# Kernel optimization log

Measured on AMD Instinct MI355X. Metric: run time of the kernel, lower is better.

## Reference

```python
import jax, jax.numpy as jnp
import numpy as np

B, T, D, H = 8, 512, 1024, 16
DK = D // H  # 64
EPS = 1e-3  # Keras BatchNormalization default epsilon


def batchnorm(x, gamma, beta):
    # Keras BN over feature axis (-1), training-mode batch statistics over (B, T)
    mean = jnp.mean(x, axis=(0, 1), keepdims=True)
    var = jnp.var(x, axis=(0, 1), keepdims=True)
    return (x - mean) * jax.lax.rsqrt(var + EPS) * gamma + beta


def setup_inputs() -> dict:
    key = jax.random.key(0)
    ks = jax.random.split(key, 12)
    s = 0.05
    return {
        "x": jax.random.normal(ks[0], (B, T, D), dtype=jnp.float32),
        "Wq": jax.random.uniform(ks[1], (H, D, DK), dtype=jnp.float32, minval=-s, maxval=s),
        "Wk": jax.random.uniform(ks[2], (H, D, DK), dtype=jnp.float32, minval=-s, maxval=s),
        "Wv": jax.random.uniform(ks[3], (H, D, DK), dtype=jnp.float32, minval=-s, maxval=s),
        "W": jax.random.uniform(ks[4], (D, D), dtype=jnp.float32, minval=-s, maxval=s),
        "W1": jax.random.normal(ks[5], (D, D), dtype=jnp.float32) * 0.02,
        "b1": jnp.zeros((D,), dtype=jnp.float32),
        "W2": jax.random.normal(ks[6], (D, D), dtype=jnp.float32) * 0.02,
        "b2": jnp.zeros((D,), dtype=jnp.float32),
        "g1": jnp.ones((D,), dtype=jnp.float32),
        "be1": jnp.zeros((D,), dtype=jnp.float32),
        "g2": jnp.ones((D,), dtype=jnp.float32),
        "be2": jnp.zeros((D,), dtype=jnp.float32),
    }


def reference(x, Wq, Wk, Wv, W, W1, b1, W2, b2, g1, be1, g2, be2):
    # Batched multi-head attention (replaces the per-head Python loop)
    q = jnp.einsum("btd,hdk->bhtk", x, Wq)
    k = jnp.einsum("btd,hdk->bhtk", x, Wk)
    v = jnp.einsum("btd,hdk->bhtk", x, Wv)
    scores = jnp.einsum("bhtk,bhsk->bhts", q, k) / jnp.sqrt(jnp.float32(DK))
    w = jax.nn.softmax(scores, axis=-1)
    attn = jnp.einsum("bhts,bhsk->bhtk", w, v)
    # concat heads: [B,H,T,DK] -> [B,T,H*DK] (head-major concat order as in the loop)
    concat = jnp.transpose(attn, (0, 2, 1, 3)).reshape(B, T, D)
    out = concat @ W
    out1 = batchnorm(x + out, g1, be1)
    out2 = jax.nn.relu(out1 @ W1 + b1) @ W2 + b2
    return batchnorm(out1 + out2, g2, be2)
```

## Files before the change

kernel.cpp:

```cpp
#include <hip/hip_runtime.h>
#include <hip/hip_bf16.h>
#include <cstdint>

#define Bn 8
#define Tn 512
#define Dn 1024
#define Hn 16
#define DKn 64
#define Mn (Bn * Tn)

typedef unsigned short u16;
typedef short bf16x8 __attribute__((ext_vector_type(8)));
typedef float f32x4 __attribute__((ext_vector_type(4)));

__device__ __forceinline__ u16 f2bf(float f) {
  unsigned int u = __builtin_bit_cast(unsigned int, f);
  u += 0x7fffu + ((u >> 16) & 1u);
  return (u16)(u >> 16);
}
__device__ __forceinline__ float bf2f(u16 v) {
  return __builtin_bit_cast(float, (unsigned int)v << 16);
}
__device__ __forceinline__ unsigned int pack2bf(float lo, float hi) {
  return (unsigned int)f2bf(lo) | ((unsigned int)f2bf(hi) << 16);
}

__device__ __forceinline__ void gl2lds16(const void* g, void* l) {
  __builtin_amdgcn_global_load_lds(
      (const __attribute__((address_space(1))) unsigned int*)g,
      (__attribute__((address_space(3))) unsigned int*)l,
      16, 0, 0);
}

__device__ __forceinline__ void bar() {
  asm volatile("" ::: "memory");
  __builtin_amdgcn_s_barrier();
  asm volatile("" ::: "memory");
}
#define WAITV(n_) asm volatile("s_waitcnt vmcnt(" #n_ ")" ::: "memory")

__global__ __launch_bounds__(256) void prep_k(
    const float* __restrict__ x, u16* __restrict__ xb,
    const float* __restrict__ wq, const float* __restrict__ wk,
    const float* __restrict__ wv, u16* __restrict__ wqkvT,
    const float* __restrict__ W, const float* __restrict__ W1,
    const float* __restrict__ W2, u16* __restrict__ wt,
    u16* __restrict__ w1t, u16* __restrict__ w2t)
{
  const int bid = blockIdx.x;
  const int t = threadIdx.x;
  if (bid < 2048) {
    const size_t i = ((size_t)bid * 256 + t) * 8;
    float4 a = *reinterpret_cast<const float4*>(&x[i]);
    float4 b = *reinterpret_cast<const float4*>(&x[i + 4]);
    uint4 w;
    w.x = pack2bf(a.x, a.y); w.y = pack2bf(a.z, a.w);
    w.z = pack2bf(b.x, b.y); w.w = pack2bf(b.z, b.w);
    *reinterpret_cast<uint4*>(&xb[i]) = w;
  } else if (bid < 2816) {
    const int idx = bid - 2048;
    const int kt = idx & 15;
    const int y  = idx >> 4;
    const int tau = y >> 4, head = y & 15;
    const float* src = (tau == 0 ? wq : tau == 1 ? wk : wv) + (size_t)head * 65536;
    const int n  = t & 63;
    const int kq = (t >> 6) << 4;
    const int k0 = kt << 6;
    u16 v[16];
#pragma unroll
    for (int j = 0; j < 16; j++)
      v[j] = f2bf(src[(size_t)(k0 + kq + j) * 64 + n]);
    u16* d = &wqkvT[((size_t)tau * 1024 + head * 64 + n) * 1024 + k0 + kq];
    *reinterpret_cast<uint4*>(&d[0]) = *reinterpret_cast<uint4*>(&v[0]);
    *reinterpret_cast<uint4*>(&d[8]) = *reinterpret_cast<uint4*>(&v[8]);
  } else {
    const int idx = bid - 2816;
    const int kt = idx & 15;
    const int rest = idx >> 4;
    const int ntl = rest & 15, z = rest >> 4;
    const float* src = (z == 0 ? W : z == 1 ? W1 : W2);
    u16* dst = (z == 0 ? wt : z == 1 ? w1t : w2t);
    const int n  = (ntl << 6) + (t & 63);
    const int kq = (t >> 6) << 4;
    const int k0 = kt << 6;
    u16 v[16];
#pragma unroll
    for (int j = 0; j < 16; j++)
      v[j] = f2bf(src[(size_t)(k0 + kq + j) * 1024 + n]);
    u16* d = &dst[(size_t)n * 1024 + k0 + kq];
    *reinterpret_cast<uint4*>(&d[0]) = *reinterpret_cast<uint4*>(&v[0]);
    *reinterpret_cast<uint4*>(&d[8]) = *reinterpret_cast<uint4*>(&v[8]);
  }
}

template<int VT>
__global__ __launch_bounds__(512) void mgemm_k(
    const u16* __restrict__ A, const u16* __restrict__ Bt,
    u16* __restrict__ Cb, int ldc, u16* __restrict__ Vt)
{
  __shared__ __align__(16) u16 As[3][4096];
  __shared__ __align__(16) u16 Bs[3][4096];

  const int nwg = gridDim.x * gridDim.y;
  const int fid = blockIdx.y * gridDim.x + blockIdx.x;
  const int lid = (fid & 7) * (nwg >> 3) + (fid >> 3);
  const int bx = lid % gridDim.x, by = lid / gridDim.x;

  const int tid  = threadIdx.x;
  const int lane = tid & 63;
  const int wid  = tid >> 6;
  const int wm = wid >> 2, wn = wid & 3;
  const int g4 = lane >> 4, r15 = lane & 15;
  const int m0 = by << 7, n0 = bx << 7;

  const int srow  = tid >> 2;
  const int sslot = tid & 3;
  const int ssw   = (srow ^ (srow >> 2)) & 3;
  const int sk8   = ((sslot ^ ssw) << 3);
  const u16* ga0 = &A[(size_t)(m0 + srow) * 1024 + sk8];
  const u16* gb0 = &Bt[(size_t)(n0 + srow) * 1024 + sk8];
  const int lofs = wid * 1024;

  f32x4 acc[4][2] = {};

  auto stage_t = [&](int t, int buf) {
    gl2lds16(ga0 + t * 32, (char*)As[buf] + lofs);
    gl2lds16(gb0 + t * 32, (char*)Bs[buf] + lofs);
  };
  auto compute_t = [&](int buf) {
    bf16x8 af[4], bfr[2];
#pragma unroll
    for (int m = 0; m < 4; m++) {
      int row = wm * 64 + m * 16 + r15;
      int sw = (row ^ (row >> 2)) & 3;
      af[m] = *reinterpret_cast<const bf16x8*>(
          (const char*)As[buf] + row * 64 + ((g4 ^ sw) << 4));
    }
#pragma unroll
    for (int n = 0; n < 2; n++) {
      int row = wn * 32 + n * 16 + r15;
      int sw = (row ^ (row >> 2)) & 3;
      bfr[n] = *reinterpret_cast<const bf16x8*>(
          (const char*)Bs[buf] + row * 64 + ((g4 ^ sw) << 4));
    }
#pragma unroll
    for (int m = 0; m < 4; m++)
#pragma unroll
      for (int n = 0; n < 2; n++)
        acc[m][n] = __builtin_amdgcn_mfma_f32_16x16x32_bf16(af[m], bfr[n], acc[m][n], 0, 0, 0);
  };

  stage_t(0, 0);
  stage_t(1, 1);

  int rd = 0, wr = 2;
#pragma unroll 1
  for (int t = 0; t < 30; ++t) {
    stage_t(t + 2, wr);
    WAITV(4);
    bar();
    compute_t(rd);
    bar();
    wr = rd;
    rd = (rd + 1 == 3) ? 0 : rd + 1;
  }
  WAITV(2);
  bar();
  compute_t(0);
  bar();
  WAITV(0);
  bar();
  compute_t(1);

  if (VT && bx >= 16) {
    bar();
    const int vcol0 = n0 - 2048;
#pragma unroll
    for (int m = 0; m < 4; m++) {
      int sloc = wm * 64 + m * 16 + g4 * 4;
#pragma unroll
      for (int n = 0; n < 2; n++) {
        int cv = wn * 32 + n * 16 + r15;
        u16* base = (cv < 64) ? (u16*)As : (u16*)Bs;
        uint2 pk;
        pk.x = pack2bf(acc[m][n][0], acc[m][n][1]);
        pk.y = pack2bf(acc[m][n][2], acc[m][n][3]);
        *reinterpret_cast<uint2*>(&base[(size_t)(cv & 63) * 136 + sloc]) = pk;
      }
    }
    bar();
    {
      int cv = tid >> 2;
      int sch = (tid & 3) << 5;
      const u16* base = (cv < 64) ? (const u16*)As : (const u16*)Bs;
      const u16* src = &base[(size_t)(cv & 63) * 136 + sch];
      uint4 v0 = *reinterpret_cast<const uint4*>(src);
      uint4 v1 = *reinterpret_cast<const uint4*>(src + 8);
      uint4 v2 = *reinterpret_cast<const uint4*>(src + 16);
      uint4 v3 = *reinterpret_cast<const uint4*>(src + 24);
      int vcol = vcol0 + cv;
      int hh = vcol >> 6, dk = vcol & 63;
      int bI = m0 >> 9, sbase = (m0 & 511) + sch;
      u16* dst = &Vt[(((size_t)(bI * 16 + hh) * 64 + dk) << 9) + sbase];
      *reinterpret_cast<uint4*>(dst) = v0;
      *reinterpret_cast<uint4*>(dst + 8) = v1;
      *reinterpret_cast<uint4*>(dst + 16) = v2;
      *reinterpret_cast<uint4*>(dst + 24) = v3;
    }
    return;
  }

#pragma unroll
  for (int m = 0; m < 4; m++) {
    int row = m0 + wm * 64 + m * 16 + g4 * 4;
#pragma unroll
    for (int n = 0; n < 2; n++) {
      int col = n0 + wn * 32 + n * 16 + r15;
#pragma unroll
      for (int j = 0; j < 4; j++)
        Cb[(size_t)(row + j) * ldc + col] = f2bf(acc[m][n][j]);
    }
  }
}

template<int BIAS, int RELU, int OUTM, int RES, int RESNORM>
__global__ __launch_bounds__(512) void mgemm64_k(
    const u16* __restrict__ A, const u16* __restrict__ Bt,
    const float* __restrict__ bias, u16* __restrict__ Cb,
    const u16* __restrict__ RresB, u16* __restrict__ Rout,
    float* __restrict__ psum, float* __restrict__ psumsq,
    const float* __restrict__ nsc, const float* __restrict__ nsh)
{
  __shared__ __align__(16) u16 As[3][2048];
  __shared__ __align__(16) u16 Bs[3][4096];

  const int nwg = gridDim.x * gridDim.y;
  const int fid = blockIdx.y * gridDim.x + blockIdx.x;
  const int lid = (fid & 7) * (nwg >> 3) + (fid >> 3);
  const int bx = lid % gridDim.x, by = lid / gridDim.x;

  const int tid  = threadIdx.x;
  const int lane = tid & 63;
  const int wid  = tid >> 6;
  const int wm = wid >> 2, wn = wid & 3;
  const int g4 = lane >> 4, r15 = lane & 15;
  const int m0 = by << 6, n0 = bx << 7;

  const int srow  = lane >> 2;
  const int sslot = lane & 3;
  const int arow  = (wid & 3) * 16 + srow;
  const int asw   = (arow ^ (arow >> 2)) & 3;
  const u16* gaP  = &A[(size_t)(m0 + arow) * 1024 + ((sslot ^ asw) << 3)];
  const int brow  = wid * 16 + srow;
  const int bsw   = (brow ^ (brow >> 2)) & 3;
  const u16* gbP  = &Bt[(size_t)(n0 + brow) * 1024 + ((sslot ^ bsw) << 3)];

  f32x4 acc[2][2] = {};

  auto stage_t = [&](int t, int buf) {
    if (wid < 4)
      gl2lds16(gaP + t * 32, (char*)As[buf] + (wid & 3) * 1024);
    gl2lds16(gbP + t * 32, (char*)Bs[buf] + wid * 1024);
  };
  auto compute_t = [&](int buf) {
    bf16x8 af[2], bfr[2];
#pragma unroll
    for (int m = 0; m < 2; m++) {
      int row = wm * 32 + m * 16 + r15;
      int sw = (row ^ (row >> 2)) & 3;
      af[m] = *reinterpret_cast<const bf16x8*>(
          (const char*)As[buf] + row * 64 + ((g4 ^ sw) << 4));
    }
#pragma unroll
    for (int n = 0; n < 2; n++) {
      int row = wn * 32 + n * 16 + r15;
      int sw = (row ^ (row >> 2)) & 3;
      bfr[n] = *reinterpret_cast<const bf16x8*>(
          (const char*)Bs[buf] + row * 64 + ((g4 ^ sw) << 4));
    }
#pragma unroll
    for (int m = 0; m < 2; m++)
#pragma unroll
      for (int n = 0; n < 2; n++)
        acc[m][n] = __builtin_amdgcn_mfma_f32_16x16x32_bf16(af[m], bfr[n], acc[m][n], 0, 0, 0);
  };

  stage_t(0, 0);
  stage_t(1, 1);

  int rd = 0, wr = 2;
#pragma unroll 1
  for (int t = 0; t < 30; ++t) {
    stage_t(t + 2, wr);
    if (wid < 4) { WAITV(4); } else { WAITV(2); }
    bar();
    compute_t(rd);
    bar();
    wr = rd;
    rd = (rd + 1 == 3) ? 0 : rd + 1;
  }
  if (wid < 4) { WAITV(2); } else { WAITV(1); }
  bar();
  compute_t(0);
  bar();
  WAITV(0);
  bar();
  compute_t(1);

  float bb[2] = {0.f, 0.f};
  if (BIAS) {
#pragma unroll
    for (int n = 0; n < 2; n++) bb[n] = bias[n0 + wn * 32 + n * 16 + r15];
  }

  if (RES) {
    float sc_[2], sh_[2];
    if (RESNORM) {
#pragma unroll
      for (int n = 0; n < 2; n++) {
        int col = n0 + wn * 32 + n * 16 + r15;
        sc_[n] = nsc[col];
        sh_[n] = nsh[col];
      }
    }
    float sp[2] = {0.f, 0.f}, sq[2] = {0.f, 0.f};
#pragma unroll
    for (int m = 0; m < 2; m++) {
      int row = m0 + wm * 32 + m * 16 + g4 * 4;
#pragma unroll
      for (int n = 0; n < 2; n++) {
        int col = n0 + wn * 32 + n * 16 + r15;
#pragma unroll
        for (int j = 0; j < 4; j++) {
          size_t off = (size_t)(row + j) * 1024 + col;
          float v = acc[m][n][j] + bb[n];
          float res = bf2f(RresB[off]);
          if (RESNORM) res = fmaf(res, sc_[n], sh_[n]);
          float r = v + res;
          Rout[off] = f2bf(r);
          sp[n] += r;
          sq[n] = fmaf(r, r, sq[n]);
        }
      }
    }
#pragma unroll
    for (int n = 0; n < 2; n++) {
      sp[n] += __shfl_xor(sp[n], 16, 64);
      sp[n] += __shfl_xor(sp[n], 32, 64);
      sq[n] += __shfl_xor(sq[n], 16, 64);
      sq[n] += __shfl_xor(sq[n], 32, 64);
    }
    if (g4 == 0) {
      int slot = (by << 1) + wm;
#pragma unroll
      for (int n = 0; n < 2; n++) {
        int col = n0 + wn * 32 + n * 16 + r15;
        psum[(size_t)slot * 1024 + col] = sp[n];
        psumsq[(size_t)slot * 1024 + col] = sq[n];
      }
    }
    return;
  }

#pragma unroll
  for (int m = 0; m < 2; m++) {
    int row = m0 + wm * 32 + m * 16 + g4 * 4;
#pragma unroll
    for (int n = 0; n < 2; n++) {
      int col = n0 + wn * 32 + n * 16 + r15;
#pragma unroll
      for (int j = 0; j < 4; j++) {
        float v = acc[m][n][j];
        if (BIAS) v += bb[n];
        if (RELU) v = fmaxf(v, 0.f);
        if (OUTM == 1) Cb[(size_t)(row + j) * 1024 + col] = f2bf(v);
      }
    }
  }
}

__global__ __launch_bounds__(256, 2) void attn_k(
    const u16* __restrict__ qk, const u16* __restrict__ Vt,
    u16* __restrict__ o)
{
  __shared__ __align__(16) unsigned char Ks[2][16384];
  __shared__ __align__(16) unsigned char Vs[2][16384];
  __shared__ __align__(16) unsigned char Ps[16384];

  const int bh  = blockIdx.x;
  const int qc  = blockIdx.y;
  const int b   = bh >> 4, h = bh & 15;
  const int tid = threadIdx.x;
  const int lane = tid & 63;
  const int wv   = tid >> 6;
  const int qcol = lane & 15;
  const int g    = lane >> 4;

  const size_t rowbase = (size_t)b * Tn;
  const size_t qrow0   = rowbase + qc * 64 + wv * 16;

  bf16x8 qf[2];
  {
    const u16* qp = &qk[(qrow0 + qcol) * 2048 + h * 64 + g * 8];
    qf[0] = *reinterpret_cast<const bf16x8*>(qp);
    qf[1] = *reinterpret_cast<const bf16x8*>(qp + 32);
  }

  f32x4 oa[4] = {};
  float m_run = -3e38f, l_run = 0.f;

  const int krow = tid >> 3, kch = tid & 7;
  const int vrow = tid >> 4, vch = tid & 15;
  unsigned char* Pw = &Ps[wv * 4096];

  auto stage_kv = [&](int c, int buf) {
#pragma unroll
    for (int i = 0; i < 4; i++) {
      int row = i * 32 + krow;
      const u16* gk = &qk[(rowbase + c * 128 + row) * 2048 + 1024 + h * 64
                          + ((kch ^ (row & 7)) << 3)];
      gl2lds16(gk, (char*)Ks[buf] + wv * 1024 + i * 4096);
    }
#pragma unroll
    for (int i = 0; i < 4; i++) {
      int row = i * 16 + vrow;
      const u16* gv = &Vt[(((size_t)bh * 64 + row) << 9) + c * 128
                          + ((vch ^ (row & 7)) << 3)];
      gl2lds16(gv, (char*)Vs[buf] + wv * 1024 + i * 4096);
    }
  };

  auto compute_c = [&](int cur) {
    f32x4 sf[8];
    __builtin_amdgcn_s_setprio(1);
#pragma unroll
    for (int t = 0; t < 8; t++) {
      sf[t] = (f32x4){0.f, 0.f, 0.f, 0.f};
      const int srow = t * 16 + qcol;
      const int base = srow * 128;
      const int sw = srow & 7;
#pragma unroll
      for (int ks = 0; ks < 2; ks++) {
        bf16x8 a = *reinterpret_cast<const bf16x8*>(
            &Ks[cur][base + (((ks * 4 + g) ^ sw) << 4)]);
        sf[t] = __builtin_amdgcn_mfma_f32_16x16x32_bf16(a, qf[ks], sf[t], 0, 0, 0);
      }
    }
    __builtin_amdgcn_s_setprio(0);

    float mc = -3e38f;
#pragma unroll
    for (int t = 0; t < 8; t++)
#pragma unroll
      for (int r = 0; r < 4; r++) {
        float s = sf[t][r] * 0.125f;
        sf[t][r] = s;
        mc = fmaxf(mc, s);
      }
    mc = fmaxf(mc, __shfl_xor(mc, 16, 64));
    mc = fmaxf(mc, __shfl_xor(mc, 32, 64));

    if (__all(mc - m_run <= 8.f)) {
      float lsum = 0.f;
#pragma unroll
      for (int t = 0; t < 8; t++)
#pragma unroll
        for (int r = 0; r < 4; r++) {
          float e = __expf(sf[t][r] - m_run);
          sf[t][r] = e;
          lsum += e;
        }
      lsum += __shfl_xor(lsum, 16, 64);
      lsum += __shfl_xor(lsum, 32, 64);
      l_run += lsum;
    } else {
      float mnew = fmaxf(m_run, mc);
      float alpha = __expf(m_run - mnew);
      m_run = mnew;
      float lsum = 0.f;
#pragma unroll
      for (int t = 0; t < 8; t++)
#pragma unroll
        for (int r = 0; r < 4; r++) {
          float e = __expf(sf[t][r] - mnew);
          sf[t][r] = e;
          lsum += e;
        }
      lsum += __shfl_xor(lsum, 16, 64);
      lsum += __shfl_xor(lsum, 32, 64);
      l_run = l_run * alpha + lsum;
#pragma unroll
      for (int j = 0; j < 4; j++) {
        float av = __shfl(alpha, (g << 4) + g * 4 + j, 64);
#pragma unroll
        for (int nt = 0; nt < 4; nt++) oa[nt][j] *= av;
      }
    }

#pragma unroll
    for (int t = 0; t < 8; t++) {
      int o0 = t * 32 + g * 8;
      int chunk = o0 >> 4;
      int sb = ((chunk ^ (qcol & 7)) << 4) | (o0 & 15);
      *reinterpret_cast<unsigned int*>(&Pw[qcol * 256 + sb]) =
          pack2bf(sf[t][0], sf[t][1]);
      *reinterpret_cast<unsigned int*>(&Pw[qcol * 256 + sb + 4]) =
          pack2bf(sf[t][2], sf[t][3]);
    }

    bf16x8 pa[4];
#pragma unroll
    for (int ks = 0; ks < 4; ks++)
      pa[ks] = *reinterpret_cast<const bf16x8*>(
          &Pw[qcol * 256 + (((ks * 4 + g) ^ (qcol & 7)) << 4)]);
    __builtin_amdgcn_s_setprio(1);
#pragma unroll
    for (int nt = 0; nt < 4; nt++) {
      const int vr = nt * 16 + qcol;
      const int vsw = vr & 7;
#pragma unroll
      for (int ks = 0; ks < 4; ks++) {
        bf16x8 bvf = *reinterpret_cast<const bf16x8*>(
            &Vs[cur][vr * 256 + (((ks * 4 + g) ^ vsw) << 4)]);
        oa[nt] = __builtin_amdgcn_mfma_f32_16x16x32_bf16(pa[ks], bvf, oa[nt], 0, 0, 0);
      }
    }
    __builtin_amdgcn_s_setprio(0);
  };

  stage_kv(0, 0);
#pragma unroll 1
  for (int c = 0; c < 3; ++c) {
    stage_kv(c + 1, (c + 1) & 1);
    WAITV(8);
    bar();
    compute_c(c & 1);
    bar();
  }
  WAITV(0);
  bar();
  compute_c(1);

  float rl = 1.f / l_run;
#pragma unroll
  for (int j = 0; j < 4; j++) {
    float il = __shfl(rl, (g << 4) + g * 4 + j, 64);
#pragma unroll
    for (int nt = 0; nt < 4; nt++)
      o[(qrow0 + g * 4 + j) * 1024 + h * 64 + nt * 16 + qcol] =
          f2bf(oa[nt][j] * il);
  }
}

__global__ __launch_bounds__(256) void reduce_stats_k(
    const float* __restrict__ ps, const float* __restrict__ pq,
    const float* __restrict__ g, const float* __restrict__ be,
    float* __restrict__ scale, float* __restrict__ shift)
{
  __shared__ float Ls[8][32], Lq[8][32];
  const int t = threadIdx.x;
  const int col = blockIdx.x * 32 + (t & 31);
  const int rg = t >> 5;
  float s = 0.f, q = 0.f;
#pragma unroll
  for (int i = 0; i < 16; i++) {
    int p = rg * 16 + i;
    s += ps[(size_t)p * Dn + col];
    q += pq[(size_t)p * Dn + col];
  }
  Ls[rg][t & 31] = s;
  Lq[rg][t & 31] = q;
  __syncthreads();
  if (t < 32) {
    float S = 0.f, Q = 0.f;
#pragma unroll
    for (int r = 0; r < 8; r++) { S += Ls[r][t]; Q += Lq[r][t]; }
    const float invn = 1.f / 4096.f;
    float mean = S * invn;
    float var = Q * invn - mean * mean;
    float inv = rsqrtf(var + 1e-3f);
    float sc = g[col] * inv;
    scale[col] = sc;
    shift[col] = be[col] - mean * sc;
  }
}

template<int OUTMODE>
__global__ __launch_bounds__(256) void norm_k(
    const u16* __restrict__ r, const float* __restrict__ scale,
    const float* __restrict__ shift, float* __restrict__ o, u16* __restrict__ ob)
{
  const size_t i8 = ((size_t)blockIdx.x * 256 + threadIdx.x) * 8;
  const int col = (int)(i8 & 1023);
  uint4 rv = *reinterpret_cast<const uint4*>(&r[i8]);
  const u16* rs = reinterpret_cast<const u16*>(&rv);
  float4 sc0 = *reinterpret_cast<const float4*>(&scale[col]);
  float4 sc1 = *reinterpret_cast<const float4*>(&scale[col + 4]);
  float4 sh0 = *reinterpret_cast<const float4*>(&shift[col]);
  float4 sh1 = *reinterpret_cast<const float4*>(&shift[col + 4]);
  const float scs[8] = {sc0.x, sc0.y, sc0.z, sc0.w, sc1.x, sc1.y, sc1.z, sc1.w};
  const float shs[8] = {sh0.x, sh0.y, sh0.z, sh0.w, sh1.x, sh1.y, sh1.z, sh1.w};
  float v[8];
#pragma unroll
  for (int j = 0; j < 8; j++)
    v[j] = fmaf(bf2f(rs[j]), scs[j], shs[j]);
  if (OUTMODE == 0) {
    float4 o0 = make_float4(v[0], v[1], v[2], v[3]);
    float4 o1 = make_float4(v[4], v[5], v[6], v[7]);
    *reinterpret_cast<float4*>(&o[i8]) = o0;
    *reinterpret_cast<float4*>(&o[i8 + 4]) = o1;
  } else {
    uint4 p;
    p.x = pack2bf(v[0], v[1]); p.y = pack2bf(v[2], v[3]);
    p.z = pack2bf(v[4], v[5]); p.w = pack2bf(v[6], v[7]);
    *reinterpret_cast<uint4*>(&ob[i8]) = p;
  }
}

extern "C" void kernel_launch(void* const* d_in, const int* in_sizes, int n_in,
                              void* d_out, int out_size, void* d_ws, size_t ws_size,
                              hipStream_t stream)
{
  const float* x   = (const float*)d_in[0];
  const float* wq  = (const float*)d_in[1];
  const float* wk  = (const float*)d_in[2];
  const float* wv  = (const float*)d_in[3];
  const float* W   = (const float*)d_in[4];
  const float* W1  = (const float*)d_in[5];
  const float* b1  = (const float*)d_in[6];
  const float* W2  = (const float*)d_in[7];
  const float* b2  = (const float*)d_in[8];
  const float* g1  = (const float*)d_in[9];
  const float* be1 = (const float*)d_in[10];
  const float* g2  = (const float*)d_in[11];
  const float* be2 = (const float*)d_in[12];

  float* out = (float*)d_out;
  float* ws  = (float*)d_ws;

  const size_t NB = (size_t)Mn * Dn;
  float* psum   = ws;
  float* psumsq = psum + 128 * Dn;
  float* scale1 = psumsq + 128 * Dn;
  float* shift1 = scale1 + Dn;
  float* scale2 = shift1 + Dn;
  float* shift2 = scale2 + Dn;
  u16* ws1b    = (u16*)(shift2 + Dn);
  u16* ws2b    = ws1b + NB;
  u16* xb      = ws2b + NB;
  u16* qkb     = xb + NB;
  u16* vtb     = qkb + 2 * NB;
  u16* concatb = vtb + NB;
  u16* wqkvT   = concatb + NB;
  u16* wt      = wqkvT + 3 * 1048576;
  u16* w1t     = wt + 1048576;
  u16* w2t     = w1t + 1048576;
  u16* out1b = qkb;
  u16* hb    = qkb + NB;

  dim3 b256(256), b512(512);

  prep_k<<<dim3(3584), b256, 0, stream>>>(x, xb, wq, wk, wv, wqkvT,
                                          W, W1, W2, wt, w1t, w2t);
  mgemm_k<1><<<dim3(24, 32), b512, 0, stream>>>(xb, wqkvT, qkb, 2048, vtb);
  attn_k<<<dim3(128, 8), b256, 0, stream>>>(qkb, vtb, concatb);
  mgemm64_k<0, 0, 2, 1, 0><<<dim3(8, 64), b512, 0, stream>>>(
      concatb, wt, nullptr, nullptr, xb, ws1b, psum, psumsq,
      nullptr, nullptr);
  reduce_stats_k<<<dim3(32), b256, 0, stream>>>(psum, psumsq, g1, be1, scale1, shift1);
  norm_k<2><<<dim3(2048), b256, 0, stream>>>(ws1b, scale1, shift1, nullptr, out1b);
  mgemm64_k<1, 1, 1, 0, 0><<<dim3(8, 64), b512, 0, stream>>>(
      out1b, w1t, b1, hb, nullptr, nullptr, nullptr, nullptr,
      nullptr, nullptr);
  mgemm64_k<1, 0, 2, 1, 1><<<dim3(8, 64), b512, 0, stream>>>(
      hb, w2t, b2, nullptr, ws1b, ws2b, psum, psumsq,
      scale1, shift1);
  reduce_stats_k<<<dim3(32), b256, 0, stream>>>(psum, psumsq, g2, be2, scale2, shift2);
  norm_k<0><<<dim3(2048), b256, 0, stream>>>(ws2b, scale2, shift2, out, nullptr);
}
```

Measured before the change: 144.8 us.

## Replace QKV GEMM with 256x256-tile double-buffered kernel with interleaved staging

Swaps the 128x128-tile QKV projection GEMM for a 256x256-tile kernel using 128 KB of LDS double-buffered at K-step 64. Each wave computes a 128x64 sub-tile. Global-to-LDS loads are interleaved between MFMA quarter-blocks, and MFMA priority is raised with setprio. The goal is to cut global/LDS traffic per FLOP and hide load latency. The trade-offs are that the V transpose now writes directly with scattered 8-byte stores instead of going through LDS, and the grid shrinks to 192 workgroups, which may underfill the CUs.

```diff
diff --git a/kernel.cpp b/kernel.cpp
--- a/kernel.cpp
+++ b/kernel.cpp
@@ -38,6 +38,7 @@
   asm volatile("" ::: "memory");
 }
 #define WAITV(n_) asm volatile("s_waitcnt vmcnt(" #n_ ")" ::: "memory")
+#define LGKM0 asm volatile("s_waitcnt lgkmcnt(0)" ::: "memory")
 
 __global__ __launch_bounds__(256) void prep_k(
     const float* __restrict__ x, u16* __restrict__ xb,
@@ -93,132 +94,152 @@
   }
 }
 
-template<int VT>
-__global__ __launch_bounds__(512) void mgemm_k(
+__global__ __launch_bounds__(512, 2) void qkv8_k(
     const u16* __restrict__ A, const u16* __restrict__ Bt,
-    u16* __restrict__ Cb, int ldc, u16* __restrict__ Vt)
+    u16* __restrict__ qkb, u16* __restrict__ vtb)
 {
-  __shared__ __align__(16) u16 As[3][4096];
-  __shared__ __align__(16) u16 Bs[3][4096];
+  __shared__ __align__(16) u16 lds[65536];
 
   const int nwg = gridDim.x * gridDim.y;
   const int fid = blockIdx.y * gridDim.x + blockIdx.x;
   const int lid = (fid & 7) * (nwg >> 3) + (fid >> 3);
-  const int bx = lid % gridDim.x, by = lid / gridDim.x;
-
-  const int tid  = threadIdx.x;
+  const int bx = lid % 12, by = lid / 12;
+  const int m0g = by << 8, n0g = bx << 8;
+
+  const int tid = threadIdx.x;
   const int lane = tid & 63;
   const int wid  = tid >> 6;
   const int wm = wid >> 2, wn = wid & 3;
   const int g4 = lane >> 4, r15 = lane & 15;
-  const int m0 = by << 7, n0 = bx << 7;
-
-  const int srow  = tid >> 2;
-  const int sslot = tid & 3;
-  const int ssw   = (srow ^ (srow >> 2)) & 3;
-  const int sk8   = ((sslot ^ ssw) << 3);
-  const u16* ga0 = &A[(size_t)(m0 + srow) * 1024 + sk8];
-  const u16* gb0 = &Bt[(size_t)(n0 + srow) * 1024 + sk8];
-  const int lofs = wid * 1024;
-
-  f32x4 acc[4][2] = {};
-
-  auto stage_t = [&](int t, int buf) {
-    gl2lds16(ga0 + t * 32, (char*)As[buf] + lofs);
-    gl2lds16(gb0 + t * 32, (char*)Bs[buf] + lofs);
-  };
-  auto compute_t = [&](int buf) {
-    bf16x8 af[4], bfr[2];
-#pragma unroll
-    for (int m = 0; m < 4; m++) {
-      int row = wm * 64 + m * 16 + r15;
-      int sw = (row ^ (row >> 2)) & 3;
-      af[m] = *reinterpret_cast<const bf16x8*>(
-          (const char*)As[buf] + row * 64 + ((g4 ^ sw) << 4));
-    }
-#pragma unroll
-    for (int n = 0; n < 2; n++) {
-      int row = wn * 32 + n * 16 + r15;
-      int sw = (row ^ (row >> 2)) & 3;
-      bfr[n] = *reinterpret_cast<const bf16x8*>(
-          (const char*)Bs[buf] + row * 64 + ((g4 ^ sw) << 4));
-    }
-#pragma unroll
-    for (int m = 0; m < 4; m++)
-#pragma unroll
-      for (int n = 0; n < 2; n++)
-        acc[m][n] = __builtin_amdgcn_mfma_f32_16x16x32_bf16(af[m], bfr[n], acc[m][n], 0, 0, 0);
-  };
-
-  stage_t(0, 0);
-  stage_t(1, 1);
-
-  int rd = 0, wr = 2;
+
+  const int srw = tid >> 3;
+  const int sch = ((tid & 7) ^ (srw & 7)) << 3;
+  const size_t aoff = (size_t)(m0g + srw) * 1024 + sch;
+  const size_t boff = (size_t)(n0g + srw) * 1024 + sch;
+  char* const ldsA = (char*)lds;
+  char* const ldsB = (char*)lds + 65536;
+  const int dofs = wid * 1024;
+
+  auto stage_a = [&](int koff, int d, int h) {
+    const u16* s0 = A + aoff + (size_t)h * 131072 + koff;
+    char* dst = ldsA + d * 32768 + h * 16384 + dofs;
+    gl2lds16(s0, dst);
+    gl2lds16(s0 + 65536, dst + 8192);
+  };
+  auto stage_b = [&](int koff, int d, int h) {
+    const u16* s0 = Bt + boff + (size_t)h * 131072 + koff;
+    char* dst = ldsB + d * 32768 + h * 16384 + dofs;
+    gl2lds16(s0, dst);
+    gl2lds16(s0 + 65536, dst + 8192);
+  };
+
+  f32x4 acc[8][4] = {};
+  bf16x8 aq[8], bq0[4], bq1[4];
+
+  auto readA = [&](int d, int mh) {
+#pragma unroll
+    for (int mp = 0; mp < 4; mp++) {
+      int row = mh * 64 + mp * 16 + r15;
+      const char* base = ldsA + d * 32768 + wm * 16384 + row * 128;
+#pragma unroll
+      for (int ks = 0; ks < 2; ks++)
+        aq[mp * 2 + ks] = *reinterpret_cast<const bf16x8*>(
+            base + (((ks * 4 + g4) ^ (row & 7)) << 4));
+    }
+  };
+  auto readB = [&](int d, int nh, bf16x8* bq) {
+#pragma unroll
+    for (int np = 0; np < 2; np++) {
+      int rowh = (wn & 1) * 64 + (nh * 2 + np) * 16 + r15;
+      const char* base = ldsB + d * 32768 + (wn >> 1) * 16384 + rowh * 128;
+#pragma unroll
+      for (int ks = 0; ks < 2; ks++)
+        bq[np * 2 + ks] = *reinterpret_cast<const bf16x8*>(
+            base + (((ks * 4 + g4) ^ (rowh & 7)) << 4));
+    }
+  };
+  auto mmaq = [&](int mh, int nh, const bf16x8* bq) {
+    __builtin_amdgcn_s_setprio(1);
+#pragma unroll
+    for (int mp = 0; mp < 4; mp++)
+#pragma unroll
+      for (int np = 0; np < 2; np++)
+#pragma unroll
+        for (int ks = 0; ks < 2; ks++)
+          acc[mh * 4 + mp][nh * 2 + np] = __builtin_amdgcn_mfma_f32_16x16x32_bf16(
+              aq[mp * 2 + ks], bq[np * 2 + ks], acc[mh * 4 + mp][nh * 2 + np], 0, 0, 0);
+    __builtin_amdgcn_s_setprio(0);
+  };
+
+  stage_b(0, 0, 0); stage_b(0, 0, 1);
+  stage_a(0, 0, 0); stage_a(0, 0, 1);
+  stage_b(64, 1, 0); stage_b(64, 1, 1);
+  WAITV(4);
+  bar();
+
 #pragma unroll 1
-  for (int t = 0; t < 30; ++t) {
-    stage_t(t + 2, wr);
-    WAITV(4);
+  for (int i = 0; i < 8; ++i) {
+    const int k1 = (2 * i + 1) * 64;
+    const int k2 = (2 * i + 2) * 64;
+    const int k3 = (2 * i + 3) * 64;
+    const bool s2 = (i < 7);
+
+    readA(0, 0); readB(0, 0, bq0);
+    stage_a(k1, 1, 0);
+    bar(); LGKM0; mmaq(0, 0, bq0); bar();
+    readB(0, 1, bq1);
+    stage_a(k1, 1, 1);
+    bar(); LGKM0; mmaq(0, 1, bq1); bar();
+    readA(0, 1);
+    if (s2) stage_b(k2, 0, 0);
+    bar(); LGKM0; mmaq(1, 0, bq0); bar();
+    if (s2) stage_b(k2, 0, 1);
+    bar(); mmaq(1, 1, bq1);
+    if (s2) { WAITV(4); } else { WAITV(0); }
     bar();
-    compute_t(rd);
+    readA(1, 0); readB(1, 0, bq0);
+    if (s2) stage_a(k2, 0, 0);
+    bar(); LGKM0; mmaq(0, 0, bq0); bar();
+    readB(1, 1, bq1);
+    if (s2) stage_a(k2, 0, 1);
+    bar(); LGKM0; mmaq(0, 1, bq1); bar();
+    readA(1, 1);
+    if (s2) stage_b(k3, 1, 0);
+    bar(); LGKM0; mmaq(1, 0, bq0); bar();
+    if (s2) stage_b(k3, 1, 1);
+    bar(); mmaq(1, 1, bq1);
+    if (s2) { WAITV(4); }
     bar();
-    wr = rd;
-    rd = (rd + 1 == 3) ? 0 : rd + 1;
-  }
-  WAITV(2);
-  bar();
-  compute_t(0);
-  bar();
-  WAITV(0);
-  bar();
-  compute_t(1);
-
-  if (VT && bx >= 16) {
-    bar();
-    const int vcol0 = n0 - 2048;
-#pragma unroll
-    for (int m = 0; m < 4; m++) {
-      int sloc = wm * 64 + m * 16 + g4 * 4;
-#pragma unroll
-      for (int n = 0; n < 2; n++) {
-        int cv = wn * 32 + n * 16 + r15;
-        u16* base = (cv < 64) ? (u16*)As : (u16*)Bs;
+  }
+
+  if (bx < 8) {
+#pragma unroll
+    for (int m = 0; m < 8; m++) {
+      int row = m0g + wm * 128 + m * 16 + g4 * 4;
+#pragma unroll
+      for (int n = 0; n < 4; n++) {
+        int col = n0g + wn * 64 + n * 16 + r15;
+#pragma unroll
+        for (int j = 0; j < 4; j++)
+          qkb[(size_t)(row + j) * 2048 + col] = f2bf(acc[m][n][j]);
+      }
+    }
+  } else {
+    const int vc0 = n0g - 2048;
+#pragma unroll
+    for (int m = 0; m < 8; m++) {
+      int srow = m0g + wm * 128 + m * 16 + g4 * 4;
+      int bI = srow >> 9, s = srow & 511;
+#pragma unroll
+      for (int n = 0; n < 4; n++) {
+        int vcol = vc0 + wn * 64 + n * 16 + r15;
+        int hh = vcol >> 6, dk = vcol & 63;
         uint2 pk;
         pk.x = pack2bf(acc[m][n][0], acc[m][n][1]);
         pk.y = pack2bf(acc[m][n][2], acc[m][n][3]);
-        *reinterpret_cast<uint2*>(&base[(size_t)(cv & 63) * 136 + sloc]) = pk;
-      }
-    }
-    bar();
-    {
-      int cv = tid >> 2;
-      int sch = (tid & 3) << 5;
-      const u16* base = (cv < 64) ? (const u16*)As : (const u16*)Bs;
-      const u16* src = &base[(size_t)(cv & 63) * 136 + sch];
-      uint4 v0 = *reinterpret_cast<const uint4*>(src);
-      uint4 v1 = *reinterpret_cast<const uint4*>(src + 8);
-      uint4 v2 = *reinterpret_cast<const uint4*>(src + 16);
-      uint4 v3 = *reinterpret_cast<const uint4*>(src + 24);
-      int vcol = vcol0 + cv;
-      int hh = vcol >> 6, dk = vcol & 63;
-      int bI = m0 >> 9, sbase = (m0 & 511) + sch;
-      u16* dst = &Vt[(((size_t)(bI * 16 + hh) * 64 + dk) << 9) + sbase];
-      *reinterpret_cast<uint4*>(dst) = v0;
-      *reinterpret_cast<uint4*>(dst + 8) = v1;
-      *reinterpret_cast<uint4*>(dst + 16) = v2;
-      *reinterpret_cast<uint4*>(dst + 24) = v3;
-    }
-    return;
-  }
-
-#pragma unroll
-  for (int m = 0; m < 4; m++) {
-    int row = m0 + wm * 64 + m * 16 + g4 * 4;
-#pragma unroll
-    for (int n = 0; n < 2; n++) {
-      int col = n0 + wn * 32 + n * 16 + r15;
-#pragma unroll
-      for (int j = 0; j < 4; j++)
-        Cb[(size_t)(row + j) * ldc + col] = f2bf(acc[m][n][j]);
+        *reinterpret_cast<uint2*>(
+            &vtb[(((size_t)(bI * 16 + hh) * 64 + dk) << 9) + s]) = pk;
+      }
     }
   }
 }
@@ -662,7 +683,7 @@
 
   prep_k<<<dim3(3584), b256, 0, stream>>>(x, xb, wq, wk, wv, wqkvT,
                                           W, W1, W2, wt, w1t, w2t);
-  mgemm_k<1><<<dim3(24, 32), b512, 0, stream>>>(xb, wqkvT, qkb, 2048, vtb);
+  qkv8_k<<<dim3(12, 16), b512, 0, stream>>>(xb, wqkvT, qkb, vtb);
   attn_k<<<dim3(128, 8), b256, 0, stream>>>(qkb, vtb, concatb);
   mgemm64_k<0, 0, 2, 1, 0><<<dim3(8, 64), b512, 0, stream>>>(
       concatb, wt, nullptr, nullptr, xb, ws1b, psum, psumsq,
```

Result: no change. 146.3 us (+1.0%).
